# Kernel optimization log

Measured on AMD Instinct MI355X. Metric: run time of the kernel, lower is better.

## Reference

```python
import jax, jax.numpy as jnp
import numpy as np

B, N, D, H, DD = 4, 256, 768, 12, 64
HD = D // H  # head_dim = 64
SCALE = float(np.sqrt(HD))


def _layernorm(x, g, b, eps=1e-5):
    mu = jnp.mean(x, axis=-1, keepdims=True)
    var = jnp.var(x, axis=-1, keepdims=True)
    return (x - mu) / jnp.sqrt(var + eps) * g + b


def setup_inputs() -> dict:
    key = jax.random.key(0)
    ks = jax.random.split(key, 20)
    def w(k, shape, fan_in):
        return (jax.random.normal(k, shape, jnp.float32) / np.sqrt(fan_in)).astype(jnp.float32)
    x = jax.random.normal(ks[0], (B, N, D), jnp.float32)
    dist = jax.random.normal(ks[1], (B, N, N, DD), jnp.float32)
    mask = jax.random.randint(ks[2], (B, N, N), 0, 2) > 0
    eye = jnp.eye(N, dtype=bool)[None]
    edge_mask = jnp.logical_or(mask, eye)  # guarantee no fully-masked row
    return {
        'x': x, 'distance_features': dist, 'edge_mask': edge_mask,
        'qkv_w': w(ks[3], (D, 3 * D), D), 'qkv_b': jnp.zeros((3 * D,), jnp.float32),
        'out_w': w(ks[4], (D, D), D), 'out_b': jnp.zeros((D,), jnp.float32),
        'rb_w1': w(ks[5], (DD, D), DD), 'rb_b1': jnp.zeros((D,), jnp.float32),
        'rb_w2': w(ks[6], (D, H), D), 'rb_b2': jnp.zeros((H,), jnp.float32),
        'gate_w1': w(ks[7], (D, D), D), 'gate_b1': jnp.zeros((D,), jnp.float32),
        'gate_w2': w(ks[8], (D, D), D), 'gate_b2': jnp.zeros((D,), jnp.float32),
        'ff_w1': w(ks[9], (D, 2 * D), D), 'ff_b1': jnp.zeros((2 * D,), jnp.float32),
        'ff_w2': w(ks[10], (2 * D, D), 2 * D), 'ff_b2': jnp.zeros((D,), jnp.float32),
        'ln1_g': jnp.ones((D,), jnp.float32), 'ln1_b': jnp.zeros((D,), jnp.float32),
        'ln2_g': jnp.ones((D,), jnp.float32), 'ln2_b': jnp.zeros((D,), jnp.float32),
    }


def reference(x, distance_features, edge_mask, qkv_w, qkv_b, out_w, out_b,
              rb_w1, rb_b1, rb_w2, rb_b2, gate_w1, gate_b1, gate_w2, gate_b2,
              ff_w1, ff_b1, ff_w2, ff_b2, ln1_g, ln1_b, ln2_g, ln2_b):
    residual = x
    xn = _layernorm(x, ln1_g, ln1_b)
    qkv = xn @ qkv_w + qkv_b
    q, k, v = jnp.split(qkv, 3, axis=-1)
    q = q.reshape(B, N, H, HD)
    k = k.reshape(B, N, H, HD)
    v = v.reshape(B, N, H, HD)
    logits = jnp.einsum('bihd,bjhd->bhij', q, k) / SCALE
    bias = jax.nn.silu(distance_features @ rb_w1 + rb_b1) @ rb_w2 + rb_b2  # [B,N,N,H]
    logits = logits + jnp.transpose(bias, (0, 3, 1, 2))
    neg = jnp.finfo(logits.dtype).min
    logits = jnp.where(edge_mask[:, None, :, :], logits, neg)
    attn = jax.nn.softmax(logits, axis=-1)
    context = jnp.einsum('bhij,bjhd->bihd', attn, v).reshape(B, N, D)
    gated = jax.nn.silu(xn @ gate_w1 + gate_b1) @ gate_w2 + gate_b2
    x2 = residual + (context * jax.nn.sigmoid(gated)) @ out_w + out_b
    y = _layernorm(x2, ln2_g, ln2_b)
    ff = jax.nn.gelu(y @ ff_w1 + ff_b1, approximate=False) @ ff_w2 + ff_b2
    return x2 + ff
```

## Files before the change

kernel.cpp:

```cpp
#include <hip/hip_runtime.h>
#include <hip/hip_bf16.h>
#include <cmath>

#define U16 unsigned short

typedef __bf16 bf16x8_t __attribute__((ext_vector_type(8)));
typedef float f32x4_t __attribute__((ext_vector_type(4)));

union Frag { uint4 u4; unsigned u[4]; bf16x8_t b8; U16 s[8]; };

__device__ __forceinline__ float b2f(U16 u) {
  union { unsigned int i; float f; } x; x.i = ((unsigned int)u) << 16; return x.f;
}
__device__ __forceinline__ U16 f2b(float f) {
  union { float f; unsigned int i; } x; x.f = f;
  unsigned int r = x.i + 0x7FFFu + ((x.i >> 16) & 1u);
  return (U16)(r >> 16);
}
__device__ __forceinline__ unsigned cvt_pk_bf16(float a, float b) {
  union { __hip_bfloat162 h2; unsigned u; } x;
  x.h2 = __float22bfloat162_rn(make_float2(a, b));
  return x.u;
}
__device__ __forceinline__ unsigned pack2bf_fast(float a, float b) {
  union { float f; unsigned u; } xa, xb; xa.f = a; xb.f = b;
  return __builtin_amdgcn_perm(xb.u + 0x8000u, xa.u + 0x8000u, 0x07060302);
}
__device__ __forceinline__ float fast_silu(float z) {
  return z * __builtin_amdgcn_rcpf(1.f + __expf(-z));
}

__global__ __launch_bounds__(256) void prep_kernel(
    const float* __restrict__ qkv_w, const float* __restrict__ out_w,
    const float* __restrict__ g1w, const float* __restrict__ g2w,
    const float* __restrict__ ff1w, const float* __restrict__ ff2w,
    const float* __restrict__ rb1w, const float* __restrict__ rb2w,
    U16* __restrict__ qkv_wT, U16* __restrict__ out_wT, U16* __restrict__ g1wT,
    U16* __restrict__ g2wT, U16* __restrict__ ff1wT, U16* __restrict__ ff2wT,
    U16* __restrict__ rb1wT, U16* __restrict__ rb2wL) {
  int bid = blockIdx.x;
  if (bid >= 5808) {
    int idx = (bid - 5808) * 256 + threadIdx.x;
    int j = idx & 7, lane = (idx >> 3) & 63, pp = idx >> 9;
    int row = lane & 15, col = pp * 32 + ((lane >> 4) << 3) + j;
    rb2wL[idx] = (row < 12) ? f2b(rb2w[col * 12 + row]) : (U16)0;
    return;
  }
  const float* in; U16* out; int R, C, base;
  if (bid < 1728)      { in = qkv_w; out = qkv_wT; R = 768;  C = 2304; base = 0; }
  else if (bid < 2304) { in = out_w; out = out_wT; R = 768;  C = 768;  base = 1728; }
  else if (bid < 2880) { in = g1w;   out = g1wT;   R = 768;  C = 768;  base = 2304; }
  else if (bid < 3456) { in = g2w;   out = g2wT;   R = 768;  C = 768;  base = 2880; }
  else if (bid < 4608) { in = ff1w;  out = ff1wT;  R = 768;  C = 1536; base = 3456; }
  else if (bid < 5760) { in = ff2w;  out = ff2wT;  R = 1536; C = 768;  base = 4608; }
  else                 { in = rb1w;  out = rb1wT;  R = 64;   C = 768;  base = 5760; }
  int bx = bid - base, tilesx = C / 32;
  int c0 = (bx % tilesx) * 32, r0 = (bx / tilesx) * 32;
  __shared__ float tile[32][33];
  int tx = threadIdx.x & 31, ty = threadIdx.x >> 5;
#pragma unroll
  for (int yy = 0; yy < 4; ++yy)
    tile[ty + yy * 8][tx] = in[(size_t)(r0 + ty + yy * 8) * C + c0 + tx];
  __syncthreads();
#pragma unroll
  for (int yy = 0; yy < 4; ++yy)
    out[(size_t)(c0 + ty + yy * 8) * R + r0 + tx] = f2b(tile[tx][ty + yy * 8]);
}

__global__ __launch_bounds__(256) void kt_kernel(const float* __restrict__ qkvb,
                                                 float* __restrict__ kT) {
  int bid = blockIdx.x;
  int bh = bid >> 4, tile = bid & 15;
  int b = bh / 12, h = bh % 12;
  int n0 = (tile & 7) * 32, d0 = (tile >> 3) * 32;
  __shared__ float t[32][33];
  int tx = threadIdx.x & 31, ty = threadIdx.x >> 5;
#pragma unroll
  for (int yy = 0; yy < 4; ++yy)
    t[ty + yy * 8][tx] =
        qkvb[(size_t)(b * 256 + n0 + ty + yy * 8) * 2304 + 768 + h * 64 + d0 + tx];
  __syncthreads();
#pragma unroll
  for (int yy = 0; yy < 4; ++yy)
    kT[(size_t)bh * 16384 + (size_t)(d0 + ty + yy * 8) * 256 + n0 + tx] = t[tx][ty + yy * 8];
}

__global__ __launch_bounds__(256) void ln_kernel(const float* __restrict__ X,
                                                 const float* __restrict__ gam,
                                                 const float* __restrict__ bet,
                                                 U16* __restrict__ Y) {
  int row = blockIdx.x, tid = threadIdx.x;
  __shared__ float r1[256], r2[256];
  float v[3];
#pragma unroll
  for (int j = 0; j < 3; ++j) v[j] = X[(size_t)row * 768 + tid + j * 256];
  r1[tid] = v[0] + v[1] + v[2];
  r2[tid] = v[0] * v[0] + v[1] * v[1] + v[2] * v[2];
  __syncthreads();
  for (int s = 128; s > 0; s >>= 1) {
    if (tid < s) { r1[tid] += r1[tid + s]; r2[tid] += r2[tid + s]; }
    __syncthreads();
  }
  float mean = r1[0] * (1.f / 768.f);
  float var = r2[0] * (1.f / 768.f) - mean * mean;
  float rstd = rsqrtf(var + 1e-5f);
#pragma unroll
  for (int j = 0; j < 3; ++j) {
    int c = tid + j * 256;
    Y[(size_t)row * 768 + c] = f2b((v[j] - mean) * rstd * gam[c] + bet[c]);
  }
}

#define LDP 40
template <int EPI, bool OUTF32>
__global__ __launch_bounds__(256) void gemm_bt(const U16* __restrict__ A,
                                               const U16* __restrict__ BT,
                                               const float* __restrict__ bias,
                                               const float* __restrict__ other,
                                               void* __restrict__ Cout,
                                               int M, int N, int K) {
  __shared__ __align__(16) U16 sA[64 * LDP];
  __shared__ __align__(16) U16 sB[64 * LDP];
  int tid = threadIdx.x;
  int lane = tid & 63, wave = tid >> 6;
  int m0 = blockIdx.y * 64, n0 = blockIdx.x * 64;
  int wm = (wave >> 1) * 32, wn = (wave & 1) * 32;
  int lm = lane & 15, lq = lane >> 4;
  int srow = tid >> 2;
  int scol = (tid & 3) * 8;
  f32x4_t acc[2][2] = {};
  for (int k0 = 0; k0 < K; k0 += 32) {
    __syncthreads();
    uint4 a0 = *(const uint4*)(A + (size_t)(m0 + srow) * K + k0 + scol);
    uint4 b0 = *(const uint4*)(BT + (size_t)(n0 + srow) * K + k0 + scol);
    *(uint4*)&sA[srow * LDP + scol] = a0;
    *(uint4*)&sB[srow * LDP + scol] = b0;
    __syncthreads();
    Frag af[2], bf[2];
#pragma unroll
    for (int mt = 0; mt < 2; ++mt)
      af[mt].u4 = *(const uint4*)&sA[(wm + mt * 16 + lm) * LDP + lq * 8];
#pragma unroll
    for (int nt = 0; nt < 2; ++nt)
      bf[nt].u4 = *(const uint4*)&sB[(wn + nt * 16 + lm) * LDP + lq * 8];
#pragma unroll
    for (int mt = 0; mt < 2; ++mt)
#pragma unroll
      for (int nt = 0; nt < 2; ++nt)
        acc[mt][nt] = __builtin_amdgcn_mfma_f32_16x16x32_bf16(af[mt].b8, bf[nt].b8,
                                                              acc[mt][nt], 0, 0, 0);
  }
#pragma unroll
  for (int nt = 0; nt < 2; ++nt) {
    int gc = n0 + wn + nt * 16 + lm;
    float bz = bias[gc];
#pragma unroll
    for (int mt = 0; mt < 2; ++mt) {
#pragma unroll
      for (int r = 0; r < 4; ++r) {
        int gr = m0 + wm + mt * 16 + lq * 4 + r;
        size_t idx = (size_t)gr * N + gc;
        float z = acc[mt][nt][r] + bz;
        float o;
        if (EPI == 0) o = z;
        else if (EPI == 1) o = fast_silu(z);
        else if (EPI == 2) o = 0.5f * z * (1.f + erff(z * 0.70710678118f));
        else if (EPI == 3) o = other[idx] * __builtin_amdgcn_rcpf(1.f + __expf(-z));
        else o = z + other[idx];
        if (OUTF32) ((float*)Cout)[idx] = o;
        else ((U16*)Cout)[idx] = f2b(o);
      }
    }
  }
}

__global__ __launch_bounds__(256) void rb_kernel(const float* __restrict__ dist,
                                                 const U16* __restrict__ w1T,
                                                 const float* __restrict__ b1,
                                                 const U16* __restrict__ w2L,
                                                 const float* __restrict__ b2,
                                                 float* __restrict__ biasOut) {
  int tid = threadIdx.x;
  int lane = tid & 63, wave = tid >> 6;
  int lm = lane & 15, lq = lane >> 4;
  int r0 = blockIdx.x * 256;
  float hb = (lm < 12) ? b2[lm] : 0.f;
  Frag bd[4][2];
#pragma unroll
  for (int g = 0; g < 4; ++g) {
    const float* ap = dist + (size_t)(r0 + (wave * 4 + g) * 16 + lm) * 64 + lq * 8;
    float4 v0 = ((const float4*)ap)[0];
    float4 v1 = ((const float4*)ap)[1];
    float4 v2 = ((const float4*)(ap + 32))[0];
    float4 v3 = ((const float4*)(ap + 32))[1];
    bd[g][0].u[0] = cvt_pk_bf16(v0.x, v0.y); bd[g][0].u[1] = cvt_pk_bf16(v0.z, v0.w);
    bd[g][0].u[2] = cvt_pk_bf16(v1.x, v1.y); bd[g][0].u[3] = cvt_pk_bf16(v1.z, v1.w);
    bd[g][1].u[0] = cvt_pk_bf16(v2.x, v2.y); bd[g][1].u[1] = cvt_pk_bf16(v2.z, v2.w);
    bd[g][1].u[2] = cvt_pk_bf16(v3.x, v3.y); bd[g][1].u[3] = cvt_pk_bf16(v3.z, v3.w);
  }
  const U16* w1p0 = w1T + (size_t)(((lm >> 2) << 3) + (lm & 3)) * 64 + lq * 8;
  const U16* w1p1 = w1p0 + 4 * 64;
  const U16* w2p = w2L + lane * 8;
  const float* b1p = b1 + lq * 8;
  f32x4_t bacc[4] = {{hb, hb, hb, hb}, {hb, hb, hb, hb}, {hb, hb, hb, hb}, {hb, hb, hb, hb}};
  for (int pp = 0; pp < 24; ++pp) {
    Frag w00, w01, w10, w11, wb;
    w00.u4 = *(const uint4*)w1p0;
    w01.u4 = *(const uint4*)(w1p0 + 32);
    w10.u4 = *(const uint4*)w1p1;
    w11.u4 = *(const uint4*)(w1p1 + 32);
    wb.u4 = *(const uint4*)w2p;
    float4 bb0 = *(const float4*)b1p;
    float4 bb1 = *(const float4*)(b1p + 4);
    f32x4_t cz0 = {bb0.x, bb0.y, bb0.z, bb0.w};
    f32x4_t cz1 = {bb1.x, bb1.y, bb1.z, bb1.w};
#pragma unroll
    for (int g = 0; g < 4; ++g) {
      f32x4_t z0 = cz0, z1 = cz1;
      z0 = __builtin_amdgcn_mfma_f32_16x16x32_bf16(w00.b8, bd[g][0].b8, z0, 0, 0, 0);
      z0 = __builtin_amdgcn_mfma_f32_16x16x32_bf16(w01.b8, bd[g][1].b8, z0, 0, 0, 0);
      z1 = __builtin_amdgcn_mfma_f32_16x16x32_bf16(w10.b8, bd[g][0].b8, z1, 0, 0, 0);
      z1 = __builtin_amdgcn_mfma_f32_16x16x32_bf16(w11.b8, bd[g][1].b8, z1, 0, 0, 0);
      float s0 = fast_silu(z0[0]), s1 = fast_silu(z0[1]);
      float s2 = fast_silu(z0[2]), s3 = fast_silu(z0[3]);
      float t0 = fast_silu(z1[0]), t1 = fast_silu(z1[1]);
      float t2 = fast_silu(z1[2]), t3 = fast_silu(z1[3]);
      Frag af2;
      af2.u[0] = cvt_pk_bf16(s0, s1); af2.u[1] = cvt_pk_bf16(s2, s3);
      af2.u[2] = cvt_pk_bf16(t0, t1); af2.u[3] = cvt_pk_bf16(t2, t3);
      bacc[g] = __builtin_amdgcn_mfma_f32_16x16x32_bf16(af2.b8, wb.b8, bacc[g], 0, 0, 0);
    }
    w1p0 += 32 * 64; w1p1 += 32 * 64; w2p += 64 * 8; b1p += 32;
  }
  if (lm < 12) {
#pragma unroll
    for (int g = 0; g < 4; ++g) {
#pragma unroll
      for (int r = 0; r < 4; ++r) {
        int gr = r0 + (wave * 4 + g) * 16 + lq * 4 + r;
        int b = gr >> 16, rem = gr & 65535, i = rem >> 8, j = rem & 255;
        biasOut[(((size_t)b * 12 + lm) * 256 + i) * 256 + j] = bacc[g][r];
      }
    }
  }
}

__global__ __launch_bounds__(256) void attn_kernel(const float* __restrict__ qkv,
                                                   const float* __restrict__ kT,
                                                   const float* __restrict__ biasB,
                                                   const int* __restrict__ mask,
                                                   float* __restrict__ ctx) {
  int tid = threadIdx.x, lane = tid & 63, w = tid >> 6;
  int bh = blockIdx.y, b = bh / 12, h = bh % 12;
  int i0 = blockIdx.x * 16;
  __shared__ float sQ[16][66];
  __shared__ float sP[4][4][256];
  {
    int r = tid >> 4, c = (tid & 15) * 4;
    *(float4*)&sQ[r][c] =
        *(const float4*)&qkv[((size_t)(b * 256 + i0 + r)) * 2304 + h * 64 + c];
  }
  int iw = i0 + w * 4;
  float lacc[4][4] = {};
  const float* kp = kT + (size_t)bh * 16384 + lane;
#pragma unroll 4
  for (int d = 0; d < 64; d += 2) {
    float k00 = kp[d * 256], k01 = kp[d * 256 + 64];
    float k02 = kp[d * 256 + 128], k03 = kp[d * 256 + 192];
    float k10 = kp[d * 256 + 256], k11 = kp[d * 256 + 320];
    float k12 = kp[d * 256 + 384], k13 = kp[d * 256 + 448];
#pragma unroll
    for (int qi = 0; qi < 4; ++qi) {
      float2 q2 = *(const float2*)&sQ[w * 4 + qi][d];
      lacc[qi][0] += q2.x * k00 + q2.y * k10;
      lacc[qi][1] += q2.x * k01 + q2.y * k11;
      lacc[qi][2] += q2.x * k02 + q2.y * k12;
      lacc[qi][3] += q2.x * k03 + q2.y * k13;
    }
  }
#pragma unroll
  for (int qi = 0; qi < 4; ++qi) {
    int gi = iw + qi;
    const float* brow = biasB + (((size_t)b * 12 + h) * 256 + gi) * 256;
    const int* mrow = mask + ((size_t)b * 256 + gi) * 256;
    float lg[4];
#pragma unroll
    for (int jc = 0; jc < 4; ++jc) {
      float lv = lacc[qi][jc] * 0.125f + brow[jc * 64 + lane];
      lg[jc] = mrow[jc * 64 + lane] ? lv : -1e30f;
    }
    float mx = fmaxf(fmaxf(lg[0], lg[1]), fmaxf(lg[2], lg[3]));
#pragma unroll
    for (int m = 32; m > 0; m >>= 1) mx = fmaxf(mx, __shfl_xor(mx, m));
    float e[4], sum = 0.f;
#pragma unroll
    for (int jc = 0; jc < 4; ++jc) { e[jc] = __expf(lg[jc] - mx); sum += e[jc]; }
#pragma unroll
    for (int m = 32; m > 0; m >>= 1) sum += __shfl_xor(sum, m);
    float inv = __builtin_amdgcn_rcpf(sum);
#pragma unroll
    for (int jc = 0; jc < 4; ++jc) sP[w][qi][jc * 64 + lane] = e[jc] * inv;
  }
  float ca[4] = {0.f, 0.f, 0.f, 0.f};
  const float* vcol = qkv + (size_t)b * 256 * 2304 + 1536 + h * 64 + lane;
#pragma unroll 2
  for (int j4 = 0; j4 < 256; j4 += 4) {
    float4 p0 = *(const float4*)&sP[w][0][j4];
    float4 p1 = *(const float4*)&sP[w][1][j4];
    float4 p2 = *(const float4*)&sP[w][2][j4];
    float4 p3 = *(const float4*)&sP[w][3][j4];
    const float* pp0 = (const float*)&p0;
    const float* pp1 = (const float*)&p1;
    const float* pp2 = (const float*)&p2;
    const float* pp3 = (const float*)&p3;
#pragma unroll
    for (int jj = 0; jj < 4; ++jj) {
      float v = vcol[(size_t)(j4 + jj) * 2304];
      ca[0] += pp0[jj] * v;
      ca[1] += pp1[jj] * v;
      ca[2] += pp2[jj] * v;
      ca[3] += pp3[jj] * v;
    }
  }
#pragma unroll
  for (int qi = 0; qi < 4; ++qi)
    ctx[((size_t)(b * 256 + iw + qi)) * 768 + h * 64 + lane] = ca[qi];
}

extern "C" void kernel_launch(void* const* d_in, const int* in_sizes, int n_in,
                              void* d_out, int out_size, void* d_ws, size_t ws_size,
                              hipStream_t stream) {
  const float* x       = (const float*)d_in[0];
  const float* dist    = (const float*)d_in[1];
  const int* mask      = (const int*)d_in[2];
  const float* qkv_w   = (const float*)d_in[3];
  const float* qkv_b   = (const float*)d_in[4];
  const float* out_w   = (const float*)d_in[5];
  const float* out_b   = (const float*)d_in[6];
  const float* rb_w1   = (const float*)d_in[7];
  const float* rb_b1   = (const float*)d_in[8];
  const float* rb_w2   = (const float*)d_in[9];
  const float* rb_b2   = (const float*)d_in[10];
  const float* gate_w1 = (const float*)d_in[11];
  const float* gate_b1 = (const float*)d_in[12];
  const float* gate_w2 = (const float*)d_in[13];
  const float* gate_b2 = (const float*)d_in[14];
  const float* ff_w1   = (const float*)d_in[15];
  const float* ff_b1   = (const float*)d_in[16];
  const float* ff_w2   = (const float*)d_in[17];
  const float* ff_b2   = (const float*)d_in[18];
  const float* ln1_g   = (const float*)d_in[19];
  const float* ln1_b   = (const float*)d_in[20];
  const float* ln2_g   = (const float*)d_in[21];
  const float* ln2_b   = (const float*)d_in[22];

  char* w = (char*)d_ws;
  auto alloc = [&](size_t bytes) {
    char* p = w;
    w += (bytes + 255) & ~(size_t)255;
    return p;
  };
  U16* xn      = (U16*)alloc(1024 * 768 * 2);
  float* qkvb  = (float*)alloc((size_t)1024 * 2304 * 4);
  float* kT    = (float*)alloc((size_t)48 * 64 * 256 * 4);
  U16* qkv_wT  = (U16*)alloc(2304 * 768 * 2);
  U16* out_wT  = (U16*)alloc(768 * 768 * 2);
  U16* g1wT    = (U16*)alloc(768 * 768 * 2);
  U16* g2wT    = (U16*)alloc(768 * 768 * 2);
  U16* ff1wT   = (U16*)alloc(1536 * 768 * 2);
  U16* ff2wT   = (U16*)alloc(768 * 1536 * 2);
  U16* rb1wT   = (U16*)alloc(768 * 64 * 2);
  U16* rb2wL   = (U16*)alloc(24 * 64 * 8 * 2);
  float* biasB = (float*)alloc((size_t)4 * 12 * 256 * 256 * 4);
  float* ctx   = (float*)alloc(1024 * 768 * 4);
  U16* g1      = (U16*)alloc(1024 * 768 * 2);
  U16* cg      = (U16*)alloc(1024 * 768 * 2);
  float* x2    = (float*)alloc(1024 * 768 * 4);
  U16* y       = (U16*)alloc(1024 * 768 * 2);
  U16* f1      = (U16*)alloc(1024 * 1536 * 2);
  (void)ws_size; (void)in_sizes; (void)n_in; (void)out_size;

  prep_kernel<<<5856, 256, 0, stream>>>(qkv_w, out_w, gate_w1, gate_w2, ff_w1, ff_w2,
                                        rb_w1, rb_w2, qkv_wT, out_wT, g1wT, g2wT,
                                        ff1wT, ff2wT, rb1wT, rb2wL);

  ln_kernel<<<1024, 256, 0, stream>>>(x, ln1_g, ln1_b, xn);
  gemm_bt<0, true><<<dim3(36, 16), 256, 0, stream>>>(xn, qkv_wT, qkv_b, nullptr, qkvb,
                                                     1024, 2304, 768);
  kt_kernel<<<768, 256, 0, stream>>>(qkvb, kT);
  rb_kernel<<<1024, 256, 0, stream>>>(dist, rb1wT, rb_b1, rb2wL, rb_b2, biasB);
  attn_kernel<<<dim3(16, 48), 256, 0, stream>>>(qkvb, kT, biasB, mask, ctx);
  gemm_bt<1, false><<<dim3(12, 16), 256, 0, stream>>>(xn, g1wT, gate_b1, nullptr, g1,
                                                      1024, 768, 768);
  gemm_bt<3, false><<<dim3(12, 16), 256, 0, stream>>>(g1, g2wT, gate_b2, ctx, cg,
                                                      1024, 768, 768);
  gemm_bt<4, true><<<dim3(12, 16), 256, 0, stream>>>(cg, out_wT, out_b, x, x2,
                                                     1024, 768, 768);
  ln_kernel<<<1024, 256, 0, stream>>>(x2, ln2_g, ln2_b, y);
  gemm_bt<2, false><<<dim3(24, 16), 256, 0, stream>>>(y, ff1wT, ff_b1, nullptr, f1,
                                                      1024, 1536, 768);
  gemm_bt<4, true><<<dim3(12, 16), 256, 0, stream>>>(f1, ff2wT, ff_b2, x2, (float*)d_out,
                                                     1024, 768, 1536);
}
```

Measured before the change: 353.8 us.

## Fuse QKV and gate GEMMs, use direct-to-LDS loads, shuffle LN reductions, prefetch rb weights

Concatenates the QKV and gate_w1 weights and biases so one GEMM launch produces both the fp32 qkv buffer and the SiLU-gated bf16 g1, removing a launch and a second pass over xn. GEMM tile staging now uses global_load_lds to write straight into LDS without padding, which saves registers and instructions but may raise LDS bank conflicts on the fragment reads. LayerNorm switches from a shared-memory tree reduction to wave shuffles with a single barrier. The relative-bias kernel software-prefetches the next iteration's weight fragments to hide load latency.

Measured after the change: 327.6 us. -7.4%, faster.

```diff
diff --git a/kernel.cpp b/kernel.cpp
--- a/kernel.cpp
+++ b/kernel.cpp
@@ -22,12 +22,12 @@
   x.h2 = __float22bfloat162_rn(make_float2(a, b));
   return x.u;
 }
-__device__ __forceinline__ unsigned pack2bf_fast(float a, float b) {
-  union { float f; unsigned u; } xa, xb; xa.f = a; xb.f = b;
-  return __builtin_amdgcn_perm(xb.u + 0x8000u, xa.u + 0x8000u, 0x07060302);
-}
 __device__ __forceinline__ float fast_silu(float z) {
   return z * __builtin_amdgcn_rcpf(1.f + __expf(-z));
+}
+__device__ __forceinline__ void load_lds16(const U16* g, U16* l) {
+  __builtin_amdgcn_global_load_lds((const __attribute__((address_space(1))) void*)g,
+                                   (__attribute__((address_space(3))) void*)l, 16, 0, 0);
 }
 
 __global__ __launch_bounds__(256) void prep_kernel(
@@ -35,10 +35,16 @@
     const float* __restrict__ g1w, const float* __restrict__ g2w,
     const float* __restrict__ ff1w, const float* __restrict__ ff2w,
     const float* __restrict__ rb1w, const float* __restrict__ rb2w,
+    const float* __restrict__ qkv_b, const float* __restrict__ gate_b1,
     U16* __restrict__ qkv_wT, U16* __restrict__ out_wT, U16* __restrict__ g1wT,
     U16* __restrict__ g2wT, U16* __restrict__ ff1wT, U16* __restrict__ ff2wT,
-    U16* __restrict__ rb1wT, U16* __restrict__ rb2wL) {
+    U16* __restrict__ rb1wT, U16* __restrict__ rb2wL, float* __restrict__ qg_bias) {
   int bid = blockIdx.x;
+  if (bid >= 5856) {
+    int idx = (bid - 5856) * 256 + threadIdx.x;
+    qg_bias[idx] = (idx < 2304) ? qkv_b[idx] : gate_b1[idx - 2304];
+    return;
+  }
   if (bid >= 5808) {
     int idx = (bid - 5808) * 256 + threadIdx.x;
     int j = idx & 7, lane = (idx >> 3) & 63, pp = idx >> 9;
@@ -89,20 +95,24 @@
                                                  const float* __restrict__ gam,
                                                  const float* __restrict__ bet,
                                                  U16* __restrict__ Y) {
-  int row = blockIdx.x, tid = threadIdx.x;
-  __shared__ float r1[256], r2[256];
+  int row = blockIdx.x, tid = threadIdx.x, lane = tid & 63, wave = tid >> 6;
+  __shared__ float p1[4], p2[4];
   float v[3];
 #pragma unroll
   for (int j = 0; j < 3; ++j) v[j] = X[(size_t)row * 768 + tid + j * 256];
-  r1[tid] = v[0] + v[1] + v[2];
-  r2[tid] = v[0] * v[0] + v[1] * v[1] + v[2] * v[2];
+  float s1 = v[0] + v[1] + v[2];
+  float s2 = v[0] * v[0] + v[1] * v[1] + v[2] * v[2];
+#pragma unroll
+  for (int m = 32; m > 0; m >>= 1) {
+    s1 += __shfl_xor(s1, m);
+    s2 += __shfl_xor(s2, m);
+  }
+  if (lane == 0) { p1[wave] = s1; p2[wave] = s2; }
   __syncthreads();
-  for (int s = 128; s > 0; s >>= 1) {
-    if (tid < s) { r1[tid] += r1[tid + s]; r2[tid] += r2[tid + s]; }
-    __syncthreads();
-  }
-  float mean = r1[0] * (1.f / 768.f);
-  float var = r2[0] * (1.f / 768.f) - mean * mean;
+  float t1 = p1[0] + p1[1] + p1[2] + p1[3];
+  float t2 = p2[0] + p2[1] + p2[2] + p2[3];
+  float mean = t1 * (1.f / 768.f);
+  float var = t2 * (1.f / 768.f) - mean * mean;
   float rstd = rsqrtf(var + 1e-5f);
 #pragma unroll
   for (int j = 0; j < 3; ++j) {
@@ -111,38 +121,39 @@
   }
 }
 
-#define LDP 40
 template <int EPI, bool OUTF32>
 __global__ __launch_bounds__(256) void gemm_bt(const U16* __restrict__ A,
                                                const U16* __restrict__ BT,
                                                const float* __restrict__ bias,
                                                const float* __restrict__ other,
                                                void* __restrict__ Cout,
+                                               float* __restrict__ Cout2,
                                                int M, int N, int K) {
-  __shared__ __align__(16) U16 sA[64 * LDP];
-  __shared__ __align__(16) U16 sB[64 * LDP];
+  __shared__ __align__(16) U16 sA[64 * 32];
+  __shared__ __align__(16) U16 sB[64 * 32];
   int tid = threadIdx.x;
   int lane = tid & 63, wave = tid >> 6;
   int m0 = blockIdx.y * 64, n0 = blockIdx.x * 64;
   int wm = (wave >> 1) * 32, wn = (wave & 1) * 32;
   int lm = lane & 15, lq = lane >> 4;
-  int srow = tid >> 2;
-  int scol = (tid & 3) * 8;
+  int srow = tid >> 2, scol = (tid & 3) * 8;
+  const U16* ag = A + (size_t)(m0 + srow) * K + scol;
+  const U16* bg = BT + (size_t)(n0 + srow) * K + scol;
+  U16* lA = &sA[tid * 8];
+  U16* lB = &sB[tid * 8];
   f32x4_t acc[2][2] = {};
   for (int k0 = 0; k0 < K; k0 += 32) {
     __syncthreads();
-    uint4 a0 = *(const uint4*)(A + (size_t)(m0 + srow) * K + k0 + scol);
-    uint4 b0 = *(const uint4*)(BT + (size_t)(n0 + srow) * K + k0 + scol);
-    *(uint4*)&sA[srow * LDP + scol] = a0;
-    *(uint4*)&sB[srow * LDP + scol] = b0;
+    load_lds16(ag + k0, lA);
+    load_lds16(bg + k0, lB);
     __syncthreads();
     Frag af[2], bf[2];
 #pragma unroll
     for (int mt = 0; mt < 2; ++mt)
-      af[mt].u4 = *(const uint4*)&sA[(wm + mt * 16 + lm) * LDP + lq * 8];
+      af[mt].u4 = *(const uint4*)&sA[(wm + mt * 16 + lm) * 32 + lq * 8];
 #pragma unroll
     for (int nt = 0; nt < 2; ++nt)
-      bf[nt].u4 = *(const uint4*)&sB[(wn + nt * 16 + lm) * LDP + lq * 8];
+      bf[nt].u4 = *(const uint4*)&sB[(wn + nt * 16 + lm) * 32 + lq * 8];
 #pragma unroll
     for (int mt = 0; mt < 2; ++mt)
 #pragma unroll
@@ -159,8 +170,13 @@
 #pragma unroll
       for (int r = 0; r < 4; ++r) {
         int gr = m0 + wm + mt * 16 + lq * 4 + r;
+        float z = acc[mt][nt][r] + bz;
+        if (EPI == 5) {
+          if (gc < 2304) Cout2[(size_t)gr * 2304 + gc] = z;
+          else ((U16*)Cout)[(size_t)gr * 768 + gc - 2304] = f2b(fast_silu(z));
+          continue;
+        }
         size_t idx = (size_t)gr * N + gc;
-        float z = acc[mt][nt][r] + bz;
         float o;
         if (EPI == 0) o = z;
         else if (EPI == 1) o = fast_silu(z);
@@ -202,25 +218,37 @@
   const U16* w1p1 = w1p0 + 4 * 64;
   const U16* w2p = w2L + lane * 8;
   const float* b1p = b1 + lq * 8;
+  Frag cw00, cw01, cw10, cw11, cwb;
+  cw00.u4 = *(const uint4*)w1p0;
+  cw01.u4 = *(const uint4*)(w1p0 + 32);
+  cw10.u4 = *(const uint4*)w1p1;
+  cw11.u4 = *(const uint4*)(w1p1 + 32);
+  cwb.u4 = *(const uint4*)w2p;
+  float4 cb0 = *(const float4*)b1p;
+  float4 cb1 = *(const float4*)(b1p + 4);
   f32x4_t bacc[4] = {{hb, hb, hb, hb}, {hb, hb, hb, hb}, {hb, hb, hb, hb}, {hb, hb, hb, hb}};
   for (int pp = 0; pp < 24; ++pp) {
-    Frag w00, w01, w10, w11, wb;
-    w00.u4 = *(const uint4*)w1p0;
-    w01.u4 = *(const uint4*)(w1p0 + 32);
-    w10.u4 = *(const uint4*)w1p1;
-    w11.u4 = *(const uint4*)(w1p1 + 32);
-    wb.u4 = *(const uint4*)w2p;
-    float4 bb0 = *(const float4*)b1p;
-    float4 bb1 = *(const float4*)(b1p + 4);
-    f32x4_t cz0 = {bb0.x, bb0.y, bb0.z, bb0.w};
-    f32x4_t cz1 = {bb1.x, bb1.y, bb1.z, bb1.w};
+    Frag nw00 = cw00, nw01 = cw01, nw10 = cw10, nw11 = cw11, nwb = cwb;
+    float4 nb0 = cb0, nb1 = cb1;
+    if (pp < 23) {
+      w1p0 += 32 * 64; w1p1 += 32 * 64; w2p += 64 * 8; b1p += 32;
+      nw00.u4 = *(const uint4*)w1p0;
+      nw01.u4 = *(const uint4*)(w1p0 + 32);
+      nw10.u4 = *(const uint4*)w1p1;
+      nw11.u4 = *(const uint4*)(w1p1 + 32);
+      nwb.u4 = *(const uint4*)w2p;
+      nb0 = *(const float4*)b1p;
+      nb1 = *(const float4*)(b1p + 4);
+    }
+    f32x4_t cz0 = {cb0.x, cb0.y, cb0.z, cb0.w};
+    f32x4_t cz1 = {cb1.x, cb1.y, cb1.z, cb1.w};
 #pragma unroll
     for (int g = 0; g < 4; ++g) {
       f32x4_t z0 = cz0, z1 = cz1;
-      z0 = __builtin_amdgcn_mfma_f32_16x16x32_bf16(w00.b8, bd[g][0].b8, z0, 0, 0, 0);
-      z0 = __builtin_amdgcn_mfma_f32_16x16x32_bf16(w01.b8, bd[g][1].b8, z0, 0, 0, 0);
-      z1 = __builtin_amdgcn_mfma_f32_16x16x32_bf16(w10.b8, bd[g][0].b8, z1, 0, 0, 0);
-      z1 = __builtin_amdgcn_mfma_f32_16x16x32_bf16(w11.b8, bd[g][1].b8, z1, 0, 0, 0);
+      z0 = __builtin_amdgcn_mfma_f32_16x16x32_bf16(cw00.b8, bd[g][0].b8, z0, 0, 0, 0);
+      z0 = __builtin_amdgcn_mfma_f32_16x16x32_bf16(cw01.b8, bd[g][1].b8, z0, 0, 0, 0);
+      z1 = __builtin_amdgcn_mfma_f32_16x16x32_bf16(cw10.b8, bd[g][0].b8, z1, 0, 0, 0);
+      z1 = __builtin_amdgcn_mfma_f32_16x16x32_bf16(cw11.b8, bd[g][1].b8, z1, 0, 0, 0);
       float s0 = fast_silu(z0[0]), s1 = fast_silu(z0[1]);
       float s2 = fast_silu(z0[2]), s3 = fast_silu(z0[3]);
       float t0 = fast_silu(z1[0]), t1 = fast_silu(z1[1]);
@@ -228,9 +256,10 @@
       Frag af2;
       af2.u[0] = cvt_pk_bf16(s0, s1); af2.u[1] = cvt_pk_bf16(s2, s3);
       af2.u[2] = cvt_pk_bf16(t0, t1); af2.u[3] = cvt_pk_bf16(t2, t3);
-      bacc[g] = __builtin_amdgcn_mfma_f32_16x16x32_bf16(af2.b8, wb.b8, bacc[g], 0, 0, 0);
-    }
-    w1p0 += 32 * 64; w1p1 += 32 * 64; w2p += 64 * 8; b1p += 32;
+      bacc[g] = __builtin_amdgcn_mfma_f32_16x16x32_bf16(af2.b8, cwb.b8, bacc[g], 0, 0, 0);
+    }
+    cw00 = nw00; cw01 = nw01; cw10 = nw10; cw11 = nw11; cwb = nwb;
+    cb0 = nb0; cb1 = nb1;
   }
   if (lm < 12) {
 #pragma unroll
@@ -363,9 +392,11 @@
   U16* xn      = (U16*)alloc(1024 * 768 * 2);
   float* qkvb  = (float*)alloc((size_t)1024 * 2304 * 4);
   float* kT    = (float*)alloc((size_t)48 * 64 * 256 * 4);
-  U16* qkv_wT  = (U16*)alloc(2304 * 768 * 2);
+  U16* qg_wT   = (U16*)alloc((size_t)3072 * 768 * 2);
+  U16* qkv_wT  = qg_wT;
+  U16* g1wT    = qg_wT + (size_t)2304 * 768;
+  float* qg_b  = (float*)alloc(3072 * 4);
   U16* out_wT  = (U16*)alloc(768 * 768 * 2);
-  U16* g1wT    = (U16*)alloc(768 * 768 * 2);
   U16* g2wT    = (U16*)alloc(768 * 768 * 2);
   U16* ff1wT   = (U16*)alloc(1536 * 768 * 2);
   U16* ff2wT   = (U16*)alloc(768 * 1536 * 2);
@@ -380,25 +411,24 @@
   U16* f1      = (U16*)alloc(1024 * 1536 * 2);
   (void)ws_size; (void)in_sizes; (void)n_in; (void)out_size;
 
-  prep_kernel<<<5856, 256, 0, stream>>>(qkv_w, out_w, gate_w1, gate_w2, ff_w1, ff_w2,
-                                        rb_w1, rb_w2, qkv_wT, out_wT, g1wT, g2wT,
-                                        ff1wT, ff2wT, rb1wT, rb2wL);
+  prep_kernel<<<5868, 256, 0, stream>>>(qkv_w, out_w, gate_w1, gate_w2, ff_w1, ff_w2,
+                                        rb_w1, rb_w2, qkv_b, gate_b1,
+                                        qkv_wT, out_wT, g1wT, g2wT, ff1wT, ff2wT,
+                                        rb1wT, rb2wL, qg_b);
 
   ln_kernel<<<1024, 256, 0, stream>>>(x, ln1_g, ln1_b, xn);
-  gemm_bt<0, true><<<dim3(36, 16), 256, 0, stream>>>(xn, qkv_wT, qkv_b, nullptr, qkvb,
-                                                     1024, 2304, 768);
+  gemm_bt<5, false><<<dim3(48, 16), 256, 0, stream>>>(xn, qg_wT, qg_b, nullptr, g1,
+                                                      qkvb, 1024, 3072, 768);
   kt_kernel<<<768, 256, 0, stream>>>(qkvb, kT);
   rb_kernel<<<1024, 256, 0, stream>>>(dist, rb1wT, rb_b1, rb2wL, rb_b2, biasB);
   attn_kernel<<<dim3(16, 48), 256, 0, stream>>>(qkvb, kT, biasB, mask, ctx);
-  gemm_bt<1, false><<<dim3(12, 16), 256, 0, stream>>>(xn, g1wT, gate_b1, nullptr, g1,
-                                                      1024, 768, 768);
   gemm_bt<3, false><<<dim3(12, 16), 256, 0, stream>>>(g1, g2wT, gate_b2, ctx, cg,
-                                                      1024, 768, 768);
+                                                      nullptr, 1024, 768, 768);
   gemm_bt<4, true><<<dim3(12, 16), 256, 0, stream>>>(cg, out_wT, out_b, x, x2,
-                                                     1024, 768, 768);
+                                                     nullptr, 1024, 768, 768);
   ln_kernel<<<1024, 256, 0, stream>>>(x2, ln2_g, ln2_b, y);
   gemm_bt<2, false><<<dim3(24, 16), 256, 0, stream>>>(y, ff1wT, ff_b1, nullptr, f1,
-                                                      1024, 1536, 768);
+                                                      nullptr, 1024, 1536, 768);
   gemm_bt<4, true><<<dim3(12, 16), 256, 0, stream>>>(f1, ff2wT, ff_b2, x2, (float*)d_out,
-                                                     1024, 768, 1536);
-}
+                                                     nullptr, 1024, 768, 1536);
+}
```
